# Performance work log

Measured on AMD Instinct MI355X. Metric: run time of the kernel, lower is better.

## Reference

```python
import jax, jax.numpy as jnp
import numpy as np

B, N, H, S = 64, 2048, 128, 8192
K, DEAD_K = 32, 8
BN_EPS = 1e-5


def _bn_train(x, gamma, beta):
    # BatchNorm1d training-mode math over (batch, length) per channel; x: [B,C,N]
    mean = jnp.mean(x, axis=(0, 2), keepdims=True)
    var = jnp.var(x, axis=(0, 2), keepdims=True)
    xh = (x - mean) * jax.lax.rsqrt(var + BN_EPS)
    return xh * gamma[None, :, None] + beta[None, :, None]


def setup_inputs() -> dict:
    key = jax.random.key(0)
    ks = jax.random.split(key, 20)

    def lin(k, out_d, in_d):
        s = 1.0 / np.sqrt(in_d)
        return jax.random.uniform(k, (out_d, in_d), jnp.float32, -s, s)

    def bias(k, d, fan_in):
        s = 1.0 / np.sqrt(fan_in)
        return jax.random.uniform(k, (d,), jnp.float32, -s, s)

    inp = {
        "pts": jax.random.normal(ks[0], (B, 3, N), jnp.float32),
        "dead_features": jax.random.randint(ks[1], (S,), 0, 10, jnp.int32),
        "conv1_w": lin(ks[2], 128, 3), "conv1_b": bias(ks[3], 128, 3),
        "conv2_w": lin(ks[4], 128, 128), "conv2_b": bias(ks[5], 128, 128),
        "conv3_w": lin(ks[6], 256, 128), "conv3_b": bias(ks[7], 256, 128),
        "conv4_w": lin(ks[8], 512, 256), "conv4_b": bias(ks[9], 512, 256),
        "bn1_g": jnp.ones(128), "bn1_b": jnp.zeros(128),
        "bn2_g": jnp.ones(128), "bn2_b": jnp.zeros(128),
        "bn3_g": jnp.ones(256), "bn3_b": jnp.zeros(256),
        "bn4_g": jnp.ones(512), "bn4_b": jnp.zeros(512),
        "fc1_w": lin(ks[10], 256, 512), "fc1_b": bias(ks[11], 256, 512),
        "fc2_w": lin(ks[12], H, 256), "fc2_b": bias(ks[13], H, 256),
        "sae2_w": lin(ks[14], H, S),  # sae1.weight = sae2.weight.T (tied init)
        "sae1_b": jnp.zeros(S), "sae2_b": jnp.zeros(H),
    }
    inp["sae1_w"] = inp["sae2_w"].T  # [S,H]
    return inp


def reference(pts, dead_features, conv1_w, conv1_b, conv2_w, conv2_b,
              conv3_w, conv3_b, conv4_w, conv4_b,
              bn1_g, bn1_b, bn2_g, bn2_b, bn3_g, bn3_b, bn4_g, bn4_b,
              fc1_w, fc1_b, fc2_w, fc2_b, sae2_w, sae1_b, sae2_b, sae1_w):
    def conv1x1(x, w, b):  # x:[B,Ci,N] w:[Co,Ci] -> [B,Co,N]
        return jnp.einsum('bcn,oc->bon', x, w) + b[None, :, None]

    h = jax.nn.relu(_bn_train(conv1x1(pts, conv1_w, conv1_b), bn1_g, bn1_b))
    h = jax.nn.relu(_bn_train(conv1x1(h, conv2_w, conv2_b), bn2_g, bn2_b))
    h = jax.nn.relu(_bn_train(conv1x1(h, conv3_w, conv3_b), bn3_g, bn3_b))
    h = _bn_train(conv1x1(h, conv4_w, conv4_b), bn4_g, bn4_b)
    h = jnp.max(h, axis=2)  # global max pool -> [B,512]
    h = jax.nn.relu(h @ fc1_w.T + fc1_b)
    x = jax.nn.relu(h @ fc2_w.T + fc2_b)  # hidden rep [B,H]

    # run_sae (stage 1, batch_topk=True)
    _x = x - sae2_b
    f = jax.nn.relu(_x @ sae1_w.T + sae1_b)  # [B,S]
    flat = f.reshape(-1)                     # [B*S]
    topk_vals, inds = jax.lax.top_k(flat, K * B)
    dead_mask = jnp.broadcast_to(dead_features >= 5, (B, S)).reshape(-1)
    dead_flat = jnp.where(dead_mask, flat, 0.0)
    dead_vals, dead_inds = jax.lax.top_k(dead_flat, DEAD_K * B)
    f_out = jnp.zeros_like(flat).at[inds].set(topk_vals).reshape(B, S)
    dead_f = jnp.zeros_like(flat).at[dead_inds].set(dead_vals).reshape(B, S)
    recon = f_out @ sae2_w.T + sae2_b
    dead_x = dead_f @ sae2_w.T + sae2_b
    return (x, recon, f_out, dead_x)
```

## Files before the change

kernel.cpp:

```cpp
#include <hip/hip_runtime.h>
#include <hip/hip_bf16.h>
#include <stdint.h>

#define B_   64
#define N_   2048
#define C1_  128
#define C2_  128
#define C3_  256
#define C4_  512
#define H_   128
#define S_   8192
#define KTOT 2048
#define DTOT 512
#define TIE_CAP 4096
#define BN_EPS 1e-5f
#define NPART 1024

#define I_PTS 0
#define I_DEAD 1
#define I_C1W 2
#define I_C1B 3
#define I_C2W 4
#define I_C2B 5
#define I_C3W 6
#define I_C3B 7
#define I_C4W 8
#define I_C4B 9
#define I_BN1G 10
#define I_BN1B 11
#define I_BN2G 12
#define I_BN2B 13
#define I_BN3G 14
#define I_BN3B 15
#define I_BN4G 16
#define I_BN4B 17
#define I_FC1W 18
#define I_FC1B 19
#define I_FC2W 20
#define I_FC2B 21
#define I_SAE2W 22
#define I_SAE1B 23
#define I_SAE2B 24
#define I_SAE1W 25

typedef const void* const* Tbl;
struct P26 { const void* p[26]; };

typedef _Float16 f16x8 __attribute__((ext_vector_type(8)));
typedef _Float16 f16x4 __attribute__((ext_vector_type(4)));
typedef float f32x16 __attribute__((ext_vector_type(16)));

__global__ void k_sentinel(float* outx, float v){
  if(threadIdx.x==0) outx[0] = v;
}

__global__ void k_route(P26 in, const void** tbl, int* flag){
  if(threadIdx.x != 0) return;
  const uint32_t* a   = (const uint32_t*)in.p[1];
  const uint32_t* g10 = (const uint32_t*)in.p[10];
  const uint32_t* d16 = (const uint32_t*)in.p[16];
  bool onesA  = a[0]==0x3F800000u && a[1]==0x3F800000u && a[2]==0x3F800000u && a[3]==0x3F800000u;
  bool intsA  = a[0]<=9u && a[1]<=9u && a[2]<=9u && a[3]<=9u;
  bool ones10 = g10[0]==0x3F800000u && g10[1]==0x3F800000u;
  bool ints16 = d16[0]<=9u && d16[1]<=9u;
  int f = 0;
  if(intsA && ones10) f = 1;
  else if(onesA && ints16) f = 2;
  const int permI[26] = {0,1,2,3,4,5,6,7,8,9,10,11,12,13,14,15,16,17,18,19,20,21,22,23,24,25};
  const int permA[26] = {21,16,9,8,11,10,13,12,15,14,1,0,3,2,5,4,7,6,18,17,20,19,25,22,24,23};
  const int* pm = (f==2) ? permA : permI;
  for(int i=0;i<26;i++) tbl[i] = in.p[pm[i]];
  *flag = f;
}

__global__ void k_init(uint32_t* ctrl, uint32_t* cnt, uint32_t* hist,
                       uint32_t* ctrl2, uint32_t* cnt2, uint32_t* hist2,
                       float* racc, float* dacc){
  int t = blockIdx.x*256 + threadIdx.x;
  if(t < 256){ hist[t]=0u; hist2[t]=0u; }
  if(t == 0){
    ctrl[0]=0u;  ctrl[1]=KTOT;  cnt[0]=0u;  cnt[1]=0u;  cnt[2]=0u;
    ctrl2[0]=0u; ctrl2[1]=DTOT; cnt2[0]=0u; cnt2[1]=0u; cnt2[2]=0u;
  }
  if(t < B_*H_){ racc[t]=0.f; dacc[t]=0.f; }
}

__global__ void k_mom(Tbl tbl, float* __restrict__ mom){
  const float* pts = (const float*)tbl[I_PTS];
  int b = blockIdx.x, t = threadIdx.x;
  const float* p0 = pts + (size_t)b*3*N_;
  const float* p1 = p0 + N_;
  const float* p2 = p1 + N_;
  float v[9] = {};
  for(int n=t;n<N_;n+=256){
    float a=p0[n], c=p1[n], d=p2[n];
    v[0]+=a; v[1]+=c; v[2]+=d;
    v[3]=fmaf(a,a,v[3]); v[4]=fmaf(a,c,v[4]); v[5]=fmaf(a,d,v[5]);
    v[6]=fmaf(c,c,v[6]); v[7]=fmaf(c,d,v[7]); v[8]=fmaf(d,d,v[8]);
  }
  __shared__ float red[256];
  for(int i=0;i<9;i++){
    red[t]=v[i]; __syncthreads();
    for(int off=128;off>0;off>>=1){ if(t<off) red[t]+=red[t+off]; __syncthreads(); }
    if(t==0) mom[b*16+i]=red[0];
    __syncthreads();
  }
}

__global__ void k_bn1fold(const float* __restrict__ mom, Tbl tbl, float* __restrict__ ew){
  const float* w1 = (const float*)tbl[I_C1W];
  const float* b1 = (const float*)tbl[I_C1B];
  const float* g  = (const float*)tbl[I_BN1G];
  const float* be = (const float*)tbl[I_BN1B];
  __shared__ float tot[9];
  int t = threadIdx.x;
  if(t < 9){
    float s=0.f;
    for(int b=0;b<B_;b++) s += mom[b*16+t];
    tot[t]=s;
  }
  __syncthreads();
  const float inv = 1.f/((float)B_*(float)N_);
  float mu0=tot[0]*inv, mu1=tot[1]*inv, mu2=tot[2]*inv;
  float M00=tot[3]*inv, M01=tot[4]*inv, M02=tot[5]*inv;
  float M11=tot[6]*inv, M12=tot[7]*inv, M22=tot[8]*inv;
  float w0=w1[t*3+0], ww1=w1[t*3+1], w2=w1[t*3+2];
  float bb=b1[t];
  float wmu = w0*mu0 + ww1*mu1 + w2*mu2;
  float m = wmu + bb;
  float E2 = w0*w0*M00 + ww1*ww1*M11 + w2*w2*M22
           + 2.f*(w0*ww1*M01 + w0*w2*M02 + ww1*w2*M12)
           + 2.f*bb*wmu + bb*bb;
  float var = E2 - m*m; if(var<0.f) var=0.f;
  float a = g[t] / sqrtf(var + BN_EPS);
  float sh = be[t] - m*a;
  ew[t*4+0]=a*w0; ew[t*4+1]=a*ww1; ew[t*4+2]=a*w2; ew[t*4+3]=fmaf(a,bb,sh);
}

template<int CI, int CO, int SRCP, int STOREY, int MM, int TILED>
__global__ __launch_bounds__(256)
void k_conv(const float* __restrict__ yin, Tbl tbl, int wi, int bi,
            const float* __restrict__ aAct, const float* __restrict__ bAct,
            float* __restrict__ yout,
            float* __restrict__ psum, float* __restrict__ psq,
            float* __restrict__ pmx, float* __restrict__ pmn){
  const float* W    = (const float*)tbl[wi];
  const float* bias = (const float*)tbl[bi];
  __shared__ float Ws[16][132];
  __shared__ float As[16][132];
  __shared__ float ps[3][128];
  const int b  = blockIdx.z;
  const int o0 = blockIdx.y*128;
  const int n0 = blockIdx.x*128;
  const int nt = blockIdx.x;
  const int t  = threadIdx.x;
  const int tx = t & 15, ty = t >> 4;
  const int wo = t >> 1;
  const int wk = (t & 1)*8;
  const int ar = t >> 4;
  const int an4 = (t & 15)*4;
  if(SRCP){
    const float* pts = (const float*)tbl[I_PTS];
    if(t < 48){
      int j = t >> 4, cc = (t & 15)*8;
      const float* pp = pts + ((size_t)b*3 + j)*N_ + n0 + cc;
      const float4 p0 = *(const float4*)pp;
      const float4 p1 = *(const float4*)(pp+4);
      ps[j][cc+0]=p0.x; ps[j][cc+1]=p0.y; ps[j][cc+2]=p0.z; ps[j][cc+3]=p0.w;
      ps[j][cc+4]=p1.x; ps[j][cc+5]=p1.y; ps[j][cc+6]=p1.z; ps[j][cc+7]=p1.w;
    }
    __syncthreads();
  }
  const float* ybase = SRCP ? (const float*)nullptr : (yin + (size_t)b*CI*N_);
  float acc[8][8] = {};
  for(int k0=0;k0<CI;k0+=16){
    {
      const float* wp = W + (size_t)(o0+wo)*CI + (k0+wk);
      const float4 wa = *(const float4*)wp;
      const float4 wb = *(const float4*)(wp+4);
      Ws[wk+0][wo]=wa.x; Ws[wk+1][wo]=wa.y; Ws[wk+2][wo]=wa.z; Ws[wk+3][wo]=wa.w;
      Ws[wk+4][wo]=wb.x; Ws[wk+5][wo]=wb.y; Ws[wk+6][wo]=wb.z; Ws[wk+7][wo]=wb.w;
    }
    {
      const int c = k0 + ar;
      float av[8];
      if(SRCP){
        const float e0=aAct[c*4+0], e1=aAct[c*4+1], e2=aAct[c*4+2], e3=aAct[c*4+3];
        #pragma unroll
        for(int x=0;x<4;x++){
          float v = fmaf(e0, ps[0][an4+x], fmaf(e1, ps[1][an4+x], fmaf(e2, ps[2][an4+x], e3)));
          av[x] = fmaxf(v, 0.f);
        }
        #pragma unroll
        for(int x=0;x<4;x++){
          float v = fmaf(e0, ps[0][64+an4+x], fmaf(e1, ps[1][64+an4+x], fmaf(e2, ps[2][64+an4+x], e3)));
          av[4+x] = fmaxf(v, 0.f);
        }
      } else {
        const float* yp = ybase + (size_t)c*N_ + n0;
        const float4 v0 = *(const float4*)(yp + an4);
        const float4 v1 = *(const float4*)(yp + 64 + an4);
        const float a = aAct[c], bb = bAct[c];
        av[0]=fmaxf(fmaf(a,v0.x,bb),0.f); av[1]=fmaxf(fmaf(a,v0.y,bb),0.f);
        av[2]=fmaxf(fmaf(a,v0.z,bb),0.f); av[3]=fmaxf(fmaf(a,v0.w,bb),0.f);
        av[4]=fmaxf(fmaf(a,v1.x,bb),0.f); av[5]=fmaxf(fmaf(a,v1.y,bb),0.f);
        av[6]=fmaxf(fmaf(a,v1.z,bb),0.f); av[7]=fmaxf(fmaf(a,v1.w,bb),0.f);
      }
      *(float4*)&As[ar][an4]    = make_float4(av[0],av[1],av[2],av[3]);
      *(float4*)&As[ar][64+an4] = make_float4(av[4],av[5],av[6],av[7]);
    }
    __syncthreads();
    #pragma unroll
    for(int kk=0;kk<16;kk++){
      const float4 w0 = *(const float4*)&Ws[kk][ty*8];
      const float4 w1 = *(const float4*)&Ws[kk][ty*8+4];
      const float4 a0 = *(const float4*)&As[kk][tx*4];
      const float4 a1 = *(const float4*)&As[kk][64+tx*4];
      const float wr[8] = {w0.x,w0.y,w0.z,w0.w,w1.x,w1.y,w1.z,w1.w};
      const float ac[8] = {a0.x,a0.y,a0.z,a0.w,a1.x,a1.y,a1.z,a1.w};
      #pragma unroll
      for(int i=0;i<8;i++)
        #pragma unroll
        for(int j=0;j<8;j++)
          acc[i][j] = fmaf(wr[i], ac[j], acc[i][j]);
    }
    __syncthreads();
  }
  float bo[8];
  #pragma unroll
  for(int i=0;i<8;i++) bo[i] = bias[o0 + ty*8 + i];
  if(STOREY && TILED){
    const int ks = (o0 + ty*8) >> 4;
    float* yb2 = yout + ((((size_t)(b*16 + nt))*(CO/16) + ks)*128)*16 + (ty&1)*8;
    #pragma unroll
    for(int jj=0;jj<8;jj++){
      const int nn = (jj<4) ? (tx*4 + jj) : (64 + tx*4 + (jj-4));
      float4 lo = make_float4(acc[0][jj]+bo[0], acc[1][jj]+bo[1],
                              acc[2][jj]+bo[2], acc[3][jj]+bo[3]);
      float4 hi = make_float4(acc[4][jj]+bo[4], acc[5][jj]+bo[5],
                              acc[6][jj]+bo[6], acc[7][jj]+bo[7]);
      *(float4*)(yb2 + (size_t)nn*16)     = lo;
      *(float4*)(yb2 + (size_t)nn*16 + 4) = hi;
    }
  }
  #pragma unroll
  for(int i=0;i<8;i++){
    const int o = o0 + ty*8 + i;
    float v[8];
    #pragma unroll
    for(int j=0;j<8;j++) v[j] = acc[i][j] + bo[i];
    if(STOREY && !TILED){
      float* yo = yout + ((size_t)b*CO + o)*N_ + n0;
      *(float4*)(yo + tx*4)      = make_float4(v[0],v[1],v[2],v[3]);
      *(float4*)(yo + 64 + tx*4) = make_float4(v[4],v[5],v[6],v[7]);
    }
    float s = 0.f, q = 0.f;
    #pragma unroll
    for(int j=0;j<8;j++){ s += v[j]; q = fmaf(v[j],v[j],q); }
    float mx=0.f, mn=0.f;
    if(MM){
      mx = v[0]; mn = v[0];
      #pragma unroll
      for(int j=1;j<8;j++){ mx = fmaxf(mx,v[j]); mn = fminf(mn,v[j]); }
    }
    #pragma unroll
    for(int m=1;m<16;m<<=1){
      s += __shfl_xor(s,m);
      q += __shfl_xor(q,m);
      if(MM){ mx = fmaxf(mx,__shfl_xor(mx,m)); mn = fminf(mn,__shfl_xor(mn,m)); }
    }
    if(tx==0){
      psum[(size_t)o*NPART + b*16 + nt] = s;
      psq [(size_t)o*NPART + b*16 + nt] = q;
      if(MM){
        pmx[((size_t)b*CO + o)*16 + nt] = mx;
        pmn[((size_t)b*CO + o)*16 + nt] = mn;
      }
    }
  }
}

__global__ void k_wcvt(Tbl tbl, _Float16* __restrict__ whi, _Float16* __restrict__ wlo){
  const float* W = (const float*)tbl[I_C4W];
  int u = blockIdx.x*256 + threadIdx.x;
  int h = u & 1, o_loc = (u>>1)&127, ks = (u>>8)&15, oy = u>>12;
  int o = oy*128 + o_loc;
  int c0 = ks*16 + h*8;
  const float* wp = W + (size_t)o*C3_ + c0;
  f16x8 vh, vl;
  #pragma unroll
  for(int j=0;j<8;j++){
    float w = wp[j]*1024.f;
    _Float16 hi = (_Float16)w;
    vh[j] = hi;
    vl[j] = (_Float16)(w - (float)hi);
  }
  int uo = (oy*16 + ks)*256 + (o_loc>>5)*64 + h*32 + (o_loc&31);
  *(f16x8*)(whi + (size_t)uo*8) = vh;
  *(f16x8*)(wlo + (size_t)uo*8) = vl;
}

__global__ void k_wcvt3(Tbl tbl, _Float16* __restrict__ whi, _Float16* __restrict__ wlo){
  const float* W = (const float*)tbl[I_C3W];
  int u = blockIdx.x*256 + threadIdx.x;
  int h = u & 1, o_loc = (u>>1)&127, ks = (u>>8)&7, oy = u>>11;
  int o = oy*128 + o_loc;
  int c0 = ks*16 + h*8;
  const float* wp = W + (size_t)o*C2_ + c0;
  f16x8 vh, vl;
  #pragma unroll
  for(int j=0;j<8;j++){
    float w = wp[j]*1024.f;
    _Float16 hi = (_Float16)w;
    vh[j] = hi;
    vl[j] = (_Float16)(w - (float)hi);
  }
  int uo = (oy*8 + ks)*256 + (o_loc>>5)*64 + h*32 + (o_loc&31);
  *(f16x8*)(whi + (size_t)uo*8) = vh;
  *(f16x8*)(wlo + (size_t)uo*8) = vl;
}

__global__ void k_t2(const float* __restrict__ y2t, const float* __restrict__ a2A,
                     const float* __restrict__ b2A,
                     _Float16* __restrict__ a2h, _Float16* __restrict__ a2l){
  int u = blockIdx.x*256 + threadIdx.x;
  int h = u & 1, nn = (u>>1)&127, ks = (u>>8)&7, tile = u>>11;
  int c0 = ks*16 + h*8;
  const float* yp = y2t + (size_t)u*8;
  f16x8 vh, vl;
  #pragma unroll
  for(int j=0;j<8;j++){
    float v = fmaxf(fmaf(a2A[c0+j], yp[j], b2A[c0+j]), 0.f);
    _Float16 hi = (_Float16)v;
    vh[j] = hi;
    vl[j] = (_Float16)(v - (float)hi);
  }
  int uo = (tile*8 + ks)*256 + (nn>>5)*64 + h*32 + (nn&31);
  *(f16x8*)(a2h + (size_t)uo*8) = vh;
  *(f16x8*)(a2l + (size_t)uo*8) = vl;
}

__global__ __launch_bounds__(256)
void k_conv3m(const _Float16* __restrict__ a2h, const _Float16* __restrict__ a2l,
              const _Float16* __restrict__ whi, const _Float16* __restrict__ wlo,
              Tbl tbl, _Float16* __restrict__ y3h, _Float16* __restrict__ y3l,
              float* __restrict__ psum, float* __restrict__ psq){
  const float* bias = (const float*)tbl[I_C3B];
  __shared__ float sred[2048];
  const int nt = blockIdx.x, oy = blockIdx.y, b = blockIdx.z;
  const int t = threadIdx.x, l = t & 63, w = t >> 6;
  const int wr = w >> 1, wc = w & 1, h = l >> 5, ln = l & 31;
  const char* gWh = (const char*)whi + (size_t)oy*32768 + wr*2048 + l*16;
  const char* gWl = (const char*)wlo + (size_t)oy*32768 + wr*2048 + l*16;
  const char* gAh = (const char*)a2h + (size_t)(b*16 + nt)*32768 + wc*2048 + l*16;
  const char* gAl = (const char*)a2l + (size_t)(b*16 + nt)*32768 + wc*2048 + l*16;
  f32x16 acc00 = {}, acc01 = {}, acc10 = {}, acc11 = {};
  f16x8 nwh0 = *(const f16x8*)(gWh);
  f16x8 nwh1 = *(const f16x8*)(gWh + 1024);
  f16x8 nwl0 = *(const f16x8*)(gWl);
  f16x8 nwl1 = *(const f16x8*)(gWl + 1024);
  f16x8 nbh0 = *(const f16x8*)(gAh);
  f16x8 nbh1 = *(const f16x8*)(gAh + 1024);
  f16x8 nbl0 = *(const f16x8*)(gAl);
  f16x8 nbl1 = *(const f16x8*)(gAl + 1024);
  #pragma unroll
  for(int ks=0; ks<8; ks++){
    f16x8 wh0 = nwh0, wh1 = nwh1, wl0 = nwl0, wl1 = nwl1;
    f16x8 bh0 = nbh0, bh1 = nbh1, bl0 = nbl0, bl1 = nbl1;
    if(ks < 7){
      const int o = (ks+1)*4096;
      nwh0 = *(const f16x8*)(gWh + o);
      nwh1 = *(const f16x8*)(gWh + o + 1024);
      nwl0 = *(const f16x8*)(gWl + o);
      nwl1 = *(const f16x8*)(gWl + o + 1024);
      nbh0 = *(const f16x8*)(gAh + o);
      nbh1 = *(const f16x8*)(gAh + o + 1024);
      nbl0 = *(const f16x8*)(gAl + o);
      nbl1 = *(const f16x8*)(gAl + o + 1024);
    }
    acc00 = __builtin_amdgcn_mfma_f32_32x32x16_f16(wh0, bh0, acc00, 0,0,0);
    acc00 = __builtin_amdgcn_mfma_f32_32x32x16_f16(wl0, bh0, acc00, 0,0,0);
    acc00 = __builtin_amdgcn_mfma_f32_32x32x16_f16(wh0, bl0, acc00, 0,0,0);
    acc01 = __builtin_amdgcn_mfma_f32_32x32x16_f16(wh0, bh1, acc01, 0,0,0);
    acc01 = __builtin_amdgcn_mfma_f32_32x32x16_f16(wl0, bh1, acc01, 0,0,0);
    acc01 = __builtin_amdgcn_mfma_f32_32x32x16_f16(wh0, bl1, acc01, 0,0,0);
    acc10 = __builtin_amdgcn_mfma_f32_32x32x16_f16(wh1, bh0, acc10, 0,0,0);
    acc10 = __builtin_amdgcn_mfma_f32_32x32x16_f16(wl1, bh0, acc10, 0,0,0);
    acc10 = __builtin_amdgcn_mfma_f32_32x32x16_f16(wh1, bl0, acc10, 0,0,0);
    acc11 = __builtin_amdgcn_mfma_f32_32x32x16_f16(wh1, bh1, acc11, 0,0,0);
    acc11 = __builtin_amdgcn_mfma_f32_32x32x16_f16(wl1, bh1, acc11, 0,0,0);
    acc11 = __builtin_amdgcn_mfma_f32_32x32x16_f16(wh1, bl1, acc11, 0,0,0);
  }
  float* Ss = sred;
  float* Sq = Ss + 1024;
  const float inv = 1.f/1024.f;
  const int o0 = oy*128;
  const int grp = ln >> 3;
  const int tile = b*16 + nt;
  #pragma unroll
  for(int to=0; to<2; to++){
    const f32x16 a0 = to ? acc10 : acc00;
    const f32x16 a1 = to ? acc11 : acc01;
    f16x4 p0h, p1h, p0l, p1l;
    #pragma unroll
    for(int r=0; r<16; r++){
      const int row = (r&3) + 8*(r>>2) + 4*h;
      const int ol = wr*64 + to*32 + row;
      const float bo = bias[o0 + ol];
      float v0 = fmaf(a0[r], inv, bo);
      float v1 = fmaf(a1[r], inv, bo);
      _Float16 h0 = (_Float16)v0, h1 = (_Float16)v1;
      p0h[r&3] = h0; p1h[r&3] = h1;
      p0l[r&3] = (_Float16)(v0 - (float)h0);
      p1l[r&3] = (_Float16)(v1 - (float)h1);
      if((r&3) == 3){
        const int o3 = o0 + wr*64 + to*32 + 8*(r>>2) + 4*h;
        const int ks3 = o3 >> 4, kk = o3 & 15;
        const int n0c = wc*64 + ln;
        const size_t rb = ((size_t)(tile*16 + ks3))*128;
        *(f16x4*)(y3h + (rb + n0c)*16 + kk)      = p0h;
        *(f16x4*)(y3h + (rb + n0c + 32)*16 + kk) = p1h;
        *(f16x4*)(y3l + (rb + n0c)*16 + kk)      = p0l;
        *(f16x4*)(y3l + (rb + n0c + 32)*16 + kk) = p1l;
      }
      float s = v0 + v1;
      float q = fmaf(v0, v0, v1*v1);
      #pragma unroll
      for(int m=1; m<8; m<<=1){
        s += __shfl_xor(s, m);
        q += __shfl_xor(q, m);
      }
      if((ln & 7) == 0){
        const int idx = (wc*4 + grp)*128 + ol;
        Ss[idx] = s;  Sq[idx] = q;
      }
    }
  }
  __syncthreads();
  if(t < 128){
    const int o = o0 + t;
    float s = 0.f, q = 0.f;
    #pragma unroll
    for(int g=0; g<8; g++){
      s += Ss[g*128 + t];
      q += Sq[g*128 + t];
    }
    psum[(size_t)o*NPART + b*16 + nt] = s;
    psq [(size_t)o*NPART + b*16 + nt] = q;
  }
}

__global__ void k_t3(const _Float16* __restrict__ y3h, const _Float16* __restrict__ y3l,
                     const float* __restrict__ a3, const float* __restrict__ b3,
                     _Float16* __restrict__ a4){
  int u = blockIdx.x*256 + threadIdx.x;
  int h = u & 1, nn = (u>>1)&127, ks = (u>>8)&15, tile = u>>12;
  int c0 = ks*16 + h*8;
  const f16x8 yh = *(const f16x8*)(y3h + (size_t)u*8);
  const f16x8 yl = *(const f16x8*)(y3l + (size_t)u*8);
  f16x8 vh;
  #pragma unroll
  for(int j=0;j<8;j++){
    float y = (float)yh[j] + (float)yl[j];
    float v = fmaxf(fmaf(a3[c0+j], y, b3[c0+j]), 0.f);
    vh[j] = (_Float16)v;
  }
  int uo = (tile*16 + ks)*256 + (nn>>5)*64 + h*32 + (nn&31);
  *(f16x8*)(a4 + (size_t)uo*8) = vh;
}

__global__ __launch_bounds__(256)
void k_conv4m(const _Float16* __restrict__ a4,
              const _Float16* __restrict__ whi, const _Float16* __restrict__ wlo,
              Tbl tbl,
              float* __restrict__ psum, float* __restrict__ psq,
              float* __restrict__ pmx, float* __restrict__ pmn){
  const float* bias = (const float*)tbl[I_C4B];
  __shared__ float sred[4096];
  const int nt = blockIdx.x, oy = blockIdx.y, b = blockIdx.z;
  const int t = threadIdx.x, l = t & 63, w = t >> 6;
  const int wr = w >> 1, wc = w & 1, h = l >> 5, ln = l & 31;
  const char* gWh = (const char*)whi + (size_t)oy*65536 + wr*2048 + l*16;
  const char* gWl = (const char*)wlo + (size_t)oy*65536 + wr*2048 + l*16;
  const char* gA  = (const char*)a4  + (size_t)(b*16 + nt)*65536 + wc*2048 + l*16;
  f32x16 acc00 = {}, acc01 = {}, acc10 = {}, acc11 = {};
  f16x8 nah0 = *(const f16x8*)(gWh);
  f16x8 nah1 = *(const f16x8*)(gWh + 1024);
  f16x8 nal0 = *(const f16x8*)(gWl);
  f16x8 nal1 = *(const f16x8*)(gWl + 1024);
  f16x8 nb0  = *(const f16x8*)(gA);
  f16x8 nb1  = *(const f16x8*)(gA + 1024);
  #pragma unroll
  for(int ks=0; ks<16; ks++){
    f16x8 ah0 = nah0, ah1 = nah1, al0 = nal0, al1 = nal1;
    f16x8 b0  = nb0,  b1  = nb1;
    if(ks < 15){
      const int o = (ks+1)*4096;
      nah0 = *(const f16x8*)(gWh + o);
      nah1 = *(const f16x8*)(gWh + o + 1024);
      nal0 = *(const f16x8*)(gWl + o);
      nal1 = *(const f16x8*)(gWl + o + 1024);
      nb0  = *(const f16x8*)(gA  + o);
      nb1  = *(const f16x8*)(gA  + o + 1024);
    }
    acc00 = __builtin_amdgcn_mfma_f32_32x32x16_f16(ah0, b0, acc00, 0,0,0);
    acc00 = __builtin_amdgcn_mfma_f32_32x32x16_f16(al0, b0, acc00, 0,0,0);
    acc01 = __builtin_amdgcn_mfma_f32_32x32x16_f16(ah0, b1, acc01, 0,0,0);
    acc01 = __builtin_amdgcn_mfma_f32_32x32x16_f16(al0, b1, acc01, 0,0,0);
    acc10 = __builtin_amdgcn_mfma_f32_32x32x16_f16(ah1, b0, acc10, 0,0,0);
    acc10 = __builtin_amdgcn_mfma_f32_32x32x16_f16(al1, b0, acc10, 0,0,0);
    acc11 = __builtin_amdgcn_mfma_f32_32x32x16_f16(ah1, b1, acc11, 0,0,0);
    acc11 = __builtin_amdgcn_mfma_f32_32x32x16_f16(al1, b1, acc11, 0,0,0);
  }
  float* Ss = sred;
  float* Sq = Ss + 1024;
  float* Sx = Sq + 1024;
  float* Sn = Sx + 1024;
  const float inv = 1.f/1024.f;
  const int o0 = oy*128;
  const int grp = ln >> 3;
  #pragma unroll
  for(int to=0; to<2; to++){
    const f32x16 a0 = to ? acc10 : acc00;
    const f32x16 a1 = to ? acc11 : acc01;
    #pragma unroll
    for(int r=0; r<16; r++){
      const int row = (r&3) + 8*(r>>2) + 4*h;
      const int ol = wr*64 + to*32 + row;
      const float bo = bias[o0 + ol];
      float v0 = fmaf(a0[r], inv, bo);
      float v1 = fmaf(a1[r], inv, bo);
      float s = v0 + v1;
      float q = fmaf(v0, v0, v1*v1);
      float mx = fmaxf(v0, v1), mn = fminf(v0, v1);
      #pragma unroll
      for(int m=1; m<8; m<<=1){
        s += __shfl_xor(s, m);
        q += __shfl_xor(q, m);
        mx = fmaxf(mx, __shfl_xor(mx, m));
        mn = fminf(mn, __shfl_xor(mn, m));
      }
      if((ln & 7) == 0){
        const int idx = (wc*4 + grp)*128 + ol;
        Ss[idx] = s;  Sq[idx] = q;
        Sx[idx] = mx; Sn[idx] = mn;
      }
    }
  }
  __syncthreads();
  if(t < 128){
    const int o = o0 + t;
    float s = 0.f, q = 0.f;
    float mx = -__builtin_inff(), mn = __builtin_inff();
    #pragma unroll
    for(int g=0; g<8; g++){
      s += Ss[g*128 + t];
      q += Sq[g*128 + t];
      mx = fmaxf(mx, Sx[g*128 + t]);
      mn = fminf(mn, Sn[g*128 + t]);
    }
    psum[(size_t)o*NPART + b*16 + nt] = s;
    psq [(size_t)o*NPART + b*16 + nt] = q;
    pmx[((size_t)b*C4_ + o)*16 + nt] = mx;
    pmn[((size_t)b*C4_ + o)*16 + nt] = mn;
  }
}

__global__ void k_finalize(const float* __restrict__ psum, const float* __restrict__ psq,
                           Tbl tbl, int gi, int bi,
                           float* __restrict__ aout, float* __restrict__ bout){
  const float* gamma = (const float*)tbl[gi];
  const float* beta  = (const float*)tbl[bi];
  int c = blockIdx.x, t = threadIdx.x;
  float s=0.f, q=0.f;
  for(int i=t;i<NPART;i+=256){ s+=psum[(size_t)c*NPART+i]; q+=psq[(size_t)c*NPART+i]; }
  __shared__ float ls[256], lq[256];
  ls[t]=s; lq[t]=q; __syncthreads();
  for(int off=128; off>0; off>>=1){
    if(t<off){ ls[t]+=ls[t+off]; lq[t]+=lq[t+off]; }
    __syncthreads();
  }
  if(t==0){
    const float cnt = (float)B_*(float)N_;
    float mean = ls[0]/cnt;
    float var  = lq[0]/cnt - mean*mean;
    if(var < 0.f) var = 0.f;
    float a = gamma[c] / sqrtf(var + BN_EPS);
    aout[c] = a;
    bout[c] = beta[c] - mean*a;
  }
}

__global__ void k_pool(const float* __restrict__ pmx, const float* __restrict__ pmn,
                       const float* __restrict__ aA, const float* __restrict__ bA,
                       float* __restrict__ pooled){
  int idx = blockIdx.x*256 + threadIdx.x;
  int o = idx & (C4_-1);
  float mx=-__builtin_inff(), mn=__builtin_inff();
  for(int k=0;k<16;k++){
    mx = fmaxf(mx, pmx[(size_t)idx*16+k]);
    mn = fminf(mn, pmn[(size_t)idx*16+k]);
  }
  float a=aA[o], bb=bA[o];
  pooled[idx] = (a>=0.f) ? fmaf(a,mx,bb) : fmaf(a,mn,bb);
}

__global__ void k_fc1(const float* __restrict__ pooled, Tbl tbl, float* __restrict__ out){
  const float* w    = (const float*)tbl[I_FC1W];
  const float* bias = (const float*)tbl[I_FC1B];
  __shared__ float xp[512];
  int b = blockIdx.x, t = threadIdx.x;
  for(int i=t;i<512;i+=256) xp[i] = pooled[(size_t)b*512+i];
  __syncthreads();
  const float* wr = w + (size_t)t*512;
  float acc = 0.f;
  for(int c=0;c<512;c++) acc = fmaf(xp[c], wr[c], acc);
  out[(size_t)b*256 + t] = fmaxf(acc + bias[t], 0.f);
}

__global__ void k_fc2(const float* __restrict__ in, Tbl tbl,
                      float* __restrict__ xbuf, float* __restrict__ xout){
  const float* w    = (const float*)tbl[I_FC2W];
  const float* bias = (const float*)tbl[I_FC2B];
  __shared__ float xp[256];
  int b = blockIdx.x, t = threadIdx.x;
  for(int i=t;i<256;i+=128) xp[i] = in[(size_t)b*256+i];
  __syncthreads();
  const float* wr = w + (size_t)t*256;
  float acc = 0.f;
  for(int c=0;c<256;c++) acc = fmaf(xp[c], wr[c], acc);
  float v = fmaxf(acc + bias[t], 0.f);
  xbuf[(size_t)b*H_ + t] = v;
  xout[(size_t)b*H_ + t] = v;
}

__global__ void k_sae(const float* __restrict__ xbuf, Tbl tbl, float* __restrict__ f){
  const float* w  = (const float*)tbl[I_SAE1W];
  const float* b1 = (const float*)tbl[I_SAE1B];
  const float* b2 = (const float*)tbl[I_SAE2B];
  __shared__ float xp[H_];
  int b = blockIdx.y, t = threadIdx.x;
  if(t < H_) xp[t] = xbuf[(size_t)b*H_ + t] - b2[t];
  __syncthreads();
  int s = blockIdx.x*256 + t;
  const float* wr = w + (size_t)s*H_;
  float acc = 0.f;
  for(int h=0;h<H_;h++) acc = fmaf(xp[h], wr[h], acc);
  acc += b1[s];
  f[(size_t)b*S_ + s] = fmaxf(acc, 0.f);
}

__global__ void k_hist(const float* __restrict__ f, Tbl tbl,
                       int mode, int shift, const uint32_t* __restrict__ ctrl,
                       uint32_t* __restrict__ hist){
  const int* df = (const int*)tbl[I_DEAD];
  __shared__ uint32_t lh[256];
  int t = threadIdx.x;
  lh[t] = 0u; __syncthreads();
  const uint32_t prefix = ctrl[0];
  const uint32_t mask = (shift == 24) ? 0u : (0xFFFFFFFFu << (shift+8));
  int i0 = blockIdx.x*1024 + t;
  #pragma unroll
  for(int j=0;j<4;j++){
    int i = i0 + j*256;
    float v = f[i];
    if(mode){ int s = i & (S_-1); if(df[s] < 5) v = 0.f; }
    uint32_t u = __float_as_uint(v);
    if((u & mask) == prefix) atomicAdd(&lh[(u>>shift)&255u], 1u);
  }
  __syncthreads();
  if(lh[t]) atomicAdd(&hist[t], lh[t]);
}

__global__ void k_scan(uint32_t* ctrl, uint32_t* hist, int shift){
  if(threadIdx.x == 0){
    uint32_t rem = ctrl[1];
    uint32_t cum = 0; int tb = 0;
    for(int bin=255; bin>=0; bin--){
      uint32_t c = hist[bin];
      if(cum + c >= rem){ tb = bin; rem = rem - cum; break; }
      cum += c;
    }
    ctrl[0] |= ((uint32_t)tb) << shift;
    ctrl[1] = rem;
  }
  __syncthreads();
  hist[threadIdx.x] = 0u;
}

__global__ void k_select(const float* __restrict__ f, Tbl tbl,
                         int mode, int kcap, const uint32_t* __restrict__ ctrl,
                         uint32_t* __restrict__ cnt, uint32_t* __restrict__ sel,
                         uint32_t* __restrict__ tie){
  const int* df = (const int*)tbl[I_DEAD];
  int i = blockIdx.x*256 + threadIdx.x;
  float v = f[i];
  if(mode){ int s = i & (S_-1); if(df[s] < 5) v = 0.f; }
  uint32_t u = __float_as_uint(v);
  const uint32_t T = ctrl[0];
  if(u > T){ uint32_t p = atomicAdd(&cnt[0], 1u); if(p < (uint32_t)kcap) sel[p] = (uint32_t)i; }
  else if(u == T){ uint32_t p = atomicAdd(&cnt[1], 1u); if(p < TIE_CAP) tie[p] = (uint32_t)i; }
}

__global__ void k_resolve(const uint32_t* __restrict__ ctrl, uint32_t* __restrict__ cnt,
                          uint32_t* __restrict__ sel, const uint32_t* __restrict__ tie,
                          int kcap){
  if(threadIdx.x != 0) return;
  uint32_t m = ctrl[1];
  uint32_t ngt = cnt[0]; if(ngt > (uint32_t)kcap) ngt = (uint32_t)kcap;
  uint32_t ntie = cnt[1]; if(ntie > TIE_CAP) ntie = TIE_CAP;
  uint32_t last = 0u; bool first = true;
  for(uint32_t it=0; it<m; it++){
    uint32_t best = 0xFFFFFFFFu;
    for(uint32_t j=0;j<ntie;j++){
      uint32_t v = tie[j];
      if((first || v > last) && v < best) best = v;
    }
    if(best == 0xFFFFFFFFu) break;
    if(ngt + it < (uint32_t)kcap) sel[ngt + it] = best;
    last = best; first = false;
  }
  uint32_t tot = ngt + m; if(tot > (uint32_t)kcap) tot = (uint32_t)kcap;
  cnt[2] = tot;
}

__global__ void k_scatter(const uint32_t* __restrict__ sel, const uint32_t* __restrict__ cnt,
                          const float* __restrict__ f, float* __restrict__ fout){
  uint32_t t = blockIdx.x*256 + threadIdx.x;
  if(t >= cnt[2]) return;
  uint32_t i = sel[t];
  if(i < (uint32_t)(B_*S_)) fout[i] = f[i];
}

__global__ void k_accum(const uint32_t* __restrict__ sel, const uint32_t* __restrict__ cnt,
                        const float* __restrict__ f, Tbl tbl, int mode,
                        float* __restrict__ acc){
  const int* df = (const int*)tbl[I_DEAD];
  const float* w2 = (const float*)tbl[I_SAE2W];
  uint32_t e = blockIdx.x;
  if(e >= cnt[2]) return;
  uint32_t i = sel[e];
  if(i >= (uint32_t)(B_*S_)) return;
  uint32_t b = i >> 13, s = i & (S_-1);
  float v = f[i];
  if(mode && df[s] < 5) v = 0.f;
  int h = threadIdx.x;
  float wv = w2[(size_t)h*S_ + s];
  atomicAdd(&acc[b*H_ + h], v*wv);
}

__global__ void k_final(const float* __restrict__ racc, const float* __restrict__ dacc,
                        Tbl tbl, float* __restrict__ outR, float* __restrict__ outD){
  const float* b2 = (const float*)tbl[I_SAE2B];
  int idx = blockIdx.x*256 + threadIdx.x;
  int h = idx & (H_-1);
  float bb = b2[h];
  outR[idx] = racc[idx] + bb;
  outD[idx] = dacc[idx] + bb;
}

__global__ void k_health(const int* __restrict__ flag, const float* __restrict__ xb,
                         float* __restrict__ outx){
  __shared__ float red[256];
  int t = threadIdx.x;
  float s = 0.f;
  for(int i=t;i<B_*H_;i+=256) s += fabsf(xb[i]);
  red[t]=s; __syncthreads();
  for(int off=128;off>0;off>>=1){ if(t<off) red[t]+=red[t+off]; __syncthreads(); }
  if(t==0){
    float avg = red[0]/(float)(B_*H_);
    int f = *flag;
    float v = 0.f;
    if(f == 0) v = 12000.f;
    else if(!(avg >= 0.05f && avg <= 50.f)) v = 40000.f + 1000.f*(float)f;
    if(v > 0.f) outx[0] = v;
  }
}

extern "C" void kernel_launch(void* const* d_in, const int* in_sizes, int n_in,
                              void* d_out, int out_size, void* d_ws, size_t ws_size,
                              hipStream_t stream){
  (void)in_sizes; (void)n_in;
  float* out       = (float*)d_out;
  float* out_x     = out;
  float* out_recon = out + 8192;
  float* out_fout  = out + 16384;
  float* out_deadx = out + 540672;

  char* p = (char*)d_ws;
  auto take = [&](size_t bytes)->char*{
    char* r = p; p += (bytes + 255) & ~(size_t)255; return r;
  };
  float* y2   = (float*)take((size_t)B_*C2_*N_*4);
  float* y3   = (float*)take((size_t)B_*C3_*N_*4);
  float* psum = (float*)take((size_t)C4_*NPART*4);
  float* psq  = (float*)take((size_t)C4_*NPART*4);
  float* pmx  = (float*)take((size_t)B_*C4_*16*4);
  float* pmn  = (float*)take((size_t)B_*C4_*16*4);
  float* mom  = (float*)take(64*16*4);
  float* ab   = (float*)take(4096*4);
  float* pooled=(float*)take((size_t)B_*C4_*4);
  float* fc1o = (float*)take((size_t)B_*256*4);
  float* xb   = (float*)take((size_t)B_*H_*4);
  float* fb   = (float*)take((size_t)B_*S_*4);
  float* racc = (float*)take((size_t)B_*H_*4);
  float* dacc = (float*)take((size_t)B_*H_*4);
  uint32_t* hist  = (uint32_t*)take(256*4);
  uint32_t* ctrl  = (uint32_t*)take(64);
  uint32_t* cnt   = (uint32_t*)take(64);
  uint32_t* sel   = (uint32_t*)take((size_t)KTOT*4);
  uint32_t* tie   = (uint32_t*)take((size_t)TIE_CAP*4);
  uint32_t* hist2 = (uint32_t*)take(256*4);
  uint32_t* ctrl2 = (uint32_t*)take(64);
  uint32_t* cnt2  = (uint32_t*)take(64);
  uint32_t* sel2  = (uint32_t*)take((size_t)DTOT*4);
  uint32_t* tie2  = (uint32_t*)take((size_t)TIE_CAP*4);
  const void** tbl = (const void**)take(32*sizeof(void*));
  int* flag = (int*)take(64);
  size_t need = (size_t)(p - (char*)d_ws);
  _Float16* y3hi = (_Float16*)y3;
  _Float16* y3lo = (_Float16*)y2;
  _Float16* a2h  = (_Float16*)((char*)y3 + 67108864);
  _Float16* a2l  = (_Float16*)((char*)y3 + 100663296);
  _Float16* a4   = (_Float16*)((char*)y3 + 67108864);
  _Float16* w4hi = (_Float16*)fb;
  _Float16* w4lo = (_Float16*)((char*)fb + 262144);
  _Float16* w3hi = (_Float16*)((char*)fb + 524288);
  _Float16* w3lo = (_Float16*)((char*)fb + 589824);

  hipMemsetAsync(d_out, 0, (size_t)out_size*sizeof(float), stream);
  if(ws_size != 0 && ws_size < need){
    k_sentinel<<<1,64,0,stream>>>(out_x, 15000.f);
    return;
  }

  P26 ptrs;
  for(int i=0;i<26;i++) ptrs.p[i] = d_in[i];
  k_route<<<1,64,0,stream>>>(ptrs, tbl, flag);
  k_init<<<32,256,0,stream>>>(ctrl,cnt,hist,ctrl2,cnt2,hist2,racc,dacc);

  k_mom<<<B_,256,0,stream>>>(tbl,mom);
  k_bn1fold<<<1,128,0,stream>>>(mom,tbl,ab);
  k_wcvt<<<64,256,0,stream>>>(tbl, w4hi, w4lo);
  k_wcvt3<<<16,256,0,stream>>>(tbl, w3hi, w3lo);

  k_conv<C1_,C2_,1,1,0,1><<<dim3(N_/128,C2_/128,B_),256,0,stream>>>(
      nullptr,tbl,I_C2W,I_C2B,ab,nullptr,y2,psum,psq,nullptr,nullptr);
  k_finalize<<<C2_,256,0,stream>>>(psum,psq,tbl,I_BN2G,I_BN2B,ab+512,ab+640);
  k_t2<<<8192,256,0,stream>>>(y2, ab+512, ab+640, a2h, a2l);
  k_conv3m<<<dim3(16,2,64),256,0,stream>>>(a2h, a2l, w3hi, w3lo, tbl,
                                           y3hi, y3lo, psum, psq);
  k_finalize<<<C3_,256,0,stream>>>(psum,psq,tbl,I_BN3G,I_BN3B,ab+768,ab+1024);
  k_t3<<<16384,256,0,stream>>>(y3hi, y3lo, ab+768, ab+1024, a4);
  k_conv4m<<<dim3(16,4,64),256,0,stream>>>(a4, w4hi, w4lo, tbl,
                                           psum, psq, pmx, pmn);
  k_finalize<<<C4_,256,0,stream>>>(psum,psq,tbl,I_BN4G,I_BN4B,ab+1280,ab+1792);
  k_pool<<<(B_*C4_)/256,256,0,stream>>>(pmx,pmn,ab+1280,ab+1792,pooled);

  k_fc1<<<B_,256,0,stream>>>(pooled,tbl,fc1o);
  k_fc2<<<B_,128,0,stream>>>(fc1o,tbl,xb,out_x);
  k_sae<<<dim3(S_/256,B_),256,0,stream>>>(xb,tbl,fb);

  for(int pass=0;pass<4;pass++){
    int shift = 24 - 8*pass;
    k_hist<<<512,256,0,stream>>>(fb,tbl,0,shift,ctrl,hist);
    k_scan<<<1,256,0,stream>>>(ctrl,hist,shift);
  }
  k_select<<<2048,256,0,stream>>>(fb,tbl,0,KTOT,ctrl,cnt,sel,tie);
  k_resolve<<<1,64,0,stream>>>(ctrl,cnt,sel,tie,KTOT);
  k_scatter<<<8,256,0,stream>>>(sel,cnt,fb,out_fout);
  k_accum<<<KTOT,128,0,stream>>>(sel,cnt,fb,tbl,0,racc);

  for(int pass=0;pass<4;pass++){
    int shift = 24 - 8*pass;
    k_hist<<<512,256,0,stream>>>(fb,tbl,1,shift,ctrl2,hist2);
    k_scan<<<1,256,0,stream>>>(ctrl2,hist2,shift);
  }
  k_select<<<2048,256,0,stream>>>(fb,tbl,1,DTOT,ctrl2,cnt2,sel2,tie2);
  k_resolve<<<1,64,0,stream>>>(ctrl2,cnt2,sel2,tie2,DTOT);
  k_accum<<<DTOT,128,0,stream>>>(sel2,cnt2,fb,tbl,1,dacc);

  k_final<<<(B_*H_)/256,256,0,stream>>>(racc,dacc,tbl,out_recon,out_deadx);

  k_health<<<1,256,0,stream>>>(flag,xb,out_x);
}
```

Baseline: 668.1 us.

## Fuse pool/fc head and run both top-k selections in shared passes

Merges the pool, fc1 and fc2 kernels into one per-batch head kernel, so the intermediate pooled and fc1 buffers no longer round-trip through global memory. The two radix-select top-k pipelines (regular and dead-feature) now run together: each histogram, scan, select, resolve and accumulate kernel handles both selections, and the scatter into f_out is folded into the accumulate kernel. This roughly halves the number of small launches and passes over the 2M-element activation buffer. In exchange each fused kernel does more work per element and uses more atomics and shared memory.

```diff
diff --git a/kernel.cpp b/kernel.cpp
--- a/kernel.cpp
+++ b/kernel.cpp
@@ -591,47 +591,44 @@
   }
 }
 
-__global__ void k_pool(const float* __restrict__ pmx, const float* __restrict__ pmn,
-                       const float* __restrict__ aA, const float* __restrict__ bA,
-                       float* __restrict__ pooled){
-  int idx = blockIdx.x*256 + threadIdx.x;
-  int o = idx & (C4_-1);
-  float mx=-__builtin_inff(), mn=__builtin_inff();
-  for(int k=0;k<16;k++){
-    mx = fmaxf(mx, pmx[(size_t)idx*16+k]);
-    mn = fminf(mn, pmn[(size_t)idx*16+k]);
-  }
-  float a=aA[o], bb=bA[o];
-  pooled[idx] = (a>=0.f) ? fmaf(a,mx,bb) : fmaf(a,mn,bb);
-}
-
-__global__ void k_fc1(const float* __restrict__ pooled, Tbl tbl, float* __restrict__ out){
-  const float* w    = (const float*)tbl[I_FC1W];
-  const float* bias = (const float*)tbl[I_FC1B];
+__global__ __launch_bounds__(256)
+void k_head(const float* __restrict__ pmx, const float* __restrict__ pmn,
+            const float* __restrict__ aA, const float* __restrict__ bA,
+            Tbl tbl, float* __restrict__ xbuf, float* __restrict__ xout){
+  const float* w1    = (const float*)tbl[I_FC1W];
+  const float* b1    = (const float*)tbl[I_FC1B];
+  const float* w2    = (const float*)tbl[I_FC2W];
+  const float* b2    = (const float*)tbl[I_FC2B];
   __shared__ float xp[512];
+  __shared__ float fo[256];
   int b = blockIdx.x, t = threadIdx.x;
-  for(int i=t;i<512;i+=256) xp[i] = pooled[(size_t)b*512+i];
+  for(int o = t; o < 512; o += 256){
+    const size_t idx = (size_t)(b*512 + o);
+    float mx=-__builtin_inff(), mn=__builtin_inff();
+    #pragma unroll
+    for(int k=0;k<16;k++){
+      mx = fmaxf(mx, pmx[idx*16+k]);
+      mn = fminf(mn, pmn[idx*16+k]);
+    }
+    float a=aA[o], bb=bA[o];
+    xp[o] = (a>=0.f) ? fmaf(a,mx,bb) : fmaf(a,mn,bb);
+  }
   __syncthreads();
-  const float* wr = w + (size_t)t*512;
-  float acc = 0.f;
-  for(int c=0;c<512;c++) acc = fmaf(xp[c], wr[c], acc);
-  out[(size_t)b*256 + t] = fmaxf(acc + bias[t], 0.f);
-}
-
-__global__ void k_fc2(const float* __restrict__ in, Tbl tbl,
-                      float* __restrict__ xbuf, float* __restrict__ xout){
-  const float* w    = (const float*)tbl[I_FC2W];
-  const float* bias = (const float*)tbl[I_FC2B];
-  __shared__ float xp[256];
-  int b = blockIdx.x, t = threadIdx.x;
-  for(int i=t;i<256;i+=128) xp[i] = in[(size_t)b*256+i];
+  {
+    const float* wr = w1 + (size_t)t*512;
+    float acc = 0.f;
+    for(int c=0;c<512;c++) acc = fmaf(xp[c], wr[c], acc);
+    fo[t] = fmaxf(acc + b1[t], 0.f);
+  }
   __syncthreads();
-  const float* wr = w + (size_t)t*256;
-  float acc = 0.f;
-  for(int c=0;c<256;c++) acc = fmaf(xp[c], wr[c], acc);
-  float v = fmaxf(acc + bias[t], 0.f);
-  xbuf[(size_t)b*H_ + t] = v;
-  xout[(size_t)b*H_ + t] = v;
+  if(t < 128){
+    const float* wr = w2 + (size_t)t*256;
+    float acc = 0.f;
+    for(int c=0;c<256;c++) acc = fmaf(fo[c], wr[c], acc);
+    float v = fmaxf(acc + b2[t], 0.f);
+    xbuf[(size_t)b*H_ + t] = v;
+    xout[(size_t)b*H_ + t] = v;
+  }
 }
 
 __global__ void k_sae(const float* __restrict__ xbuf, Tbl tbl, float* __restrict__ f){
@@ -650,62 +647,73 @@
   f[(size_t)b*S_ + s] = fmaxf(acc, 0.f);
 }
 
-__global__ void k_hist(const float* __restrict__ f, Tbl tbl,
-                       int mode, int shift, const uint32_t* __restrict__ ctrl,
-                       uint32_t* __restrict__ hist){
+__global__ void k_hist2(const float* __restrict__ f, Tbl tbl, int shift,
+                        const uint32_t* __restrict__ ctrl,  uint32_t* __restrict__ hist,
+                        const uint32_t* __restrict__ ctrl2, uint32_t* __restrict__ hist2){
   const int* df = (const int*)tbl[I_DEAD];
-  __shared__ uint32_t lh[256];
+  __shared__ uint32_t lh[256], lh2[256];
   int t = threadIdx.x;
-  lh[t] = 0u; __syncthreads();
-  const uint32_t prefix = ctrl[0];
+  lh[t] = 0u; lh2[t] = 0u; __syncthreads();
+  const uint32_t p1 = ctrl[0], p2 = ctrl2[0];
   const uint32_t mask = (shift == 24) ? 0u : (0xFFFFFFFFu << (shift+8));
   int i0 = blockIdx.x*1024 + t;
   #pragma unroll
   for(int j=0;j<4;j++){
     int i = i0 + j*256;
     float v = f[i];
-    if(mode){ int s = i & (S_-1); if(df[s] < 5) v = 0.f; }
     uint32_t u = __float_as_uint(v);
-    if((u & mask) == prefix) atomicAdd(&lh[(u>>shift)&255u], 1u);
+    if((u & mask) == p1) atomicAdd(&lh[(u>>shift)&255u], 1u);
+    int s = i & (S_-1);
+    uint32_t ud = (df[s] < 5) ? 0u : u;
+    if((ud & mask) == p2) atomicAdd(&lh2[(ud>>shift)&255u], 1u);
   }
   __syncthreads();
-  if(lh[t]) atomicAdd(&hist[t], lh[t]);
-}
-
-__global__ void k_scan(uint32_t* ctrl, uint32_t* hist, int shift){
-  if(threadIdx.x == 0){
-    uint32_t rem = ctrl[1];
-    uint32_t cum = 0; int tb = 0;
-    for(int bin=255; bin>=0; bin--){
-      uint32_t c = hist[bin];
-      if(cum + c >= rem){ tb = bin; rem = rem - cum; break; }
-      cum += c;
-    }
-    ctrl[0] |= ((uint32_t)tb) << shift;
-    ctrl[1] = rem;
-  }
+  if(lh[t])  atomicAdd(&hist[t],  lh[t]);
+  if(lh2[t]) atomicAdd(&hist2[t], lh2[t]);
+}
+
+__device__ void scan1(uint32_t* ctrl, const uint32_t* hist, int shift){
+  uint32_t rem = ctrl[1];
+  uint32_t cum = 0; int tb = 0;
+  for(int bin=255; bin>=0; bin--){
+    uint32_t c = hist[bin];
+    if(cum + c >= rem){ tb = bin; rem = rem - cum; break; }
+    cum += c;
+  }
+  ctrl[0] |= ((uint32_t)tb) << shift;
+  ctrl[1] = rem;
+}
+
+__global__ void k_scan2(uint32_t* ctrl, uint32_t* hist,
+                        uint32_t* ctrl2, uint32_t* hist2, int shift){
+  int t = threadIdx.x;
+  if(t == 0)  scan1(ctrl,  hist,  shift);
+  if(t == 64) scan1(ctrl2, hist2, shift);
   __syncthreads();
-  hist[threadIdx.x] = 0u;
-}
-
-__global__ void k_select(const float* __restrict__ f, Tbl tbl,
-                         int mode, int kcap, const uint32_t* __restrict__ ctrl,
-                         uint32_t* __restrict__ cnt, uint32_t* __restrict__ sel,
-                         uint32_t* __restrict__ tie){
+  hist[t] = 0u; hist2[t] = 0u;
+}
+
+__global__ void k_select2(const float* __restrict__ f, Tbl tbl,
+                          const uint32_t* __restrict__ ctrl,  uint32_t* __restrict__ cnt,
+                          uint32_t* __restrict__ sel,  uint32_t* __restrict__ tie,
+                          const uint32_t* __restrict__ ctrl2, uint32_t* __restrict__ cnt2,
+                          uint32_t* __restrict__ sel2, uint32_t* __restrict__ tie2){
   const int* df = (const int*)tbl[I_DEAD];
   int i = blockIdx.x*256 + threadIdx.x;
   float v = f[i];
-  if(mode){ int s = i & (S_-1); if(df[s] < 5) v = 0.f; }
   uint32_t u = __float_as_uint(v);
   const uint32_t T = ctrl[0];
-  if(u > T){ uint32_t p = atomicAdd(&cnt[0], 1u); if(p < (uint32_t)kcap) sel[p] = (uint32_t)i; }
+  if(u > T){ uint32_t p = atomicAdd(&cnt[0], 1u); if(p < (uint32_t)KTOT) sel[p] = (uint32_t)i; }
   else if(u == T){ uint32_t p = atomicAdd(&cnt[1], 1u); if(p < TIE_CAP) tie[p] = (uint32_t)i; }
-}
-
-__global__ void k_resolve(const uint32_t* __restrict__ ctrl, uint32_t* __restrict__ cnt,
-                          uint32_t* __restrict__ sel, const uint32_t* __restrict__ tie,
-                          int kcap){
-  if(threadIdx.x != 0) return;
+  int s = i & (S_-1);
+  uint32_t ud = (df[s] < 5) ? 0u : u;
+  const uint32_t T2 = ctrl2[0];
+  if(ud > T2){ uint32_t p = atomicAdd(&cnt2[0], 1u); if(p < (uint32_t)DTOT) sel2[p] = (uint32_t)i; }
+  else if(ud == T2){ uint32_t p = atomicAdd(&cnt2[1], 1u); if(p < TIE_CAP) tie2[p] = (uint32_t)i; }
+}
+
+__device__ void resolve1(const uint32_t* ctrl, uint32_t* cnt, uint32_t* sel,
+                         const uint32_t* tie, int kcap){
   uint32_t m = ctrl[1];
   uint32_t ngt = cnt[0]; if(ngt > (uint32_t)kcap) ngt = (uint32_t)kcap;
   uint32_t ntie = cnt[1]; if(ntie > TIE_CAP) ntie = TIE_CAP;
@@ -724,26 +732,37 @@
   cnt[2] = tot;
 }
 
-__global__ void k_scatter(const uint32_t* __restrict__ sel, const uint32_t* __restrict__ cnt,
-                          const float* __restrict__ f, float* __restrict__ fout){
-  uint32_t t = blockIdx.x*256 + threadIdx.x;
-  if(t >= cnt[2]) return;
-  uint32_t i = sel[t];
-  if(i < (uint32_t)(B_*S_)) fout[i] = f[i];
-}
-
-__global__ void k_accum(const uint32_t* __restrict__ sel, const uint32_t* __restrict__ cnt,
-                        const float* __restrict__ f, Tbl tbl, int mode,
-                        float* __restrict__ acc){
+__global__ void k_resolve2(const uint32_t* __restrict__ ctrl,  uint32_t* __restrict__ cnt,
+                           uint32_t* __restrict__ sel,  const uint32_t* __restrict__ tie,
+                           const uint32_t* __restrict__ ctrl2, uint32_t* __restrict__ cnt2,
+                           uint32_t* __restrict__ sel2, const uint32_t* __restrict__ tie2){
+  int t = threadIdx.x;
+  if(t == 0)  resolve1(ctrl,  cnt,  sel,  tie,  KTOT);
+  if(t == 64) resolve1(ctrl2, cnt2, sel2, tie2, DTOT);
+}
+
+__global__ void k_accum2(const uint32_t* __restrict__ sel,  const uint32_t* __restrict__ cnt,
+                         const uint32_t* __restrict__ sel2, const uint32_t* __restrict__ cnt2,
+                         const float* __restrict__ f, Tbl tbl,
+                         float* __restrict__ racc, float* __restrict__ dacc,
+                         float* __restrict__ fout){
   const int* df = (const int*)tbl[I_DEAD];
   const float* w2 = (const float*)tbl[I_SAE2W];
   uint32_t e = blockIdx.x;
-  if(e >= cnt[2]) return;
-  uint32_t i = sel[e];
-  if(i >= (uint32_t)(B_*S_)) return;
-  uint32_t b = i >> 13, s = i & (S_-1);
-  float v = f[i];
+  int mode; uint32_t idx; float* acc;
+  if(e < (uint32_t)KTOT){
+    if(e >= cnt[2]) return;
+    idx = sel[e]; mode = 0; acc = racc;
+  } else {
+    e -= (uint32_t)KTOT;
+    if(e >= cnt2[2]) return;
+    idx = sel2[e]; mode = 1; acc = dacc;
+  }
+  if(idx >= (uint32_t)(B_*S_)) return;
+  uint32_t b = idx >> 13, s = idx & (S_-1);
+  float v = f[idx];
   if(mode && df[s] < 5) v = 0.f;
+  if(mode == 0 && threadIdx.x == 0) fout[idx] = v;
   int h = threadIdx.x;
   float wv = w2[(size_t)h*S_ + s];
   atomicAdd(&acc[b*H_ + h], v*wv);
@@ -818,6 +837,7 @@
   const void** tbl = (const void**)take(32*sizeof(void*));
   int* flag = (int*)take(64);
   size_t need = (size_t)(p - (char*)d_ws);
+  (void)pooled; (void)fc1o;
   _Float16* y3hi = (_Float16*)y3;
   _Float16* y3lo = (_Float16*)y2;
   _Float16* a2h  = (_Float16*)((char*)y3 + 67108864);
@@ -855,30 +875,18 @@
   k_conv4m<<<dim3(16,4,64),256,0,stream>>>(a4, w4hi, w4lo, tbl,
                                            psum, psq, pmx, pmn);
   k_finalize<<<C4_,256,0,stream>>>(psum,psq,tbl,I_BN4G,I_BN4B,ab+1280,ab+1792);
-  k_pool<<<(B_*C4_)/256,256,0,stream>>>(pmx,pmn,ab+1280,ab+1792,pooled);
-
-  k_fc1<<<B_,256,0,stream>>>(pooled,tbl,fc1o);
-  k_fc2<<<B_,128,0,stream>>>(fc1o,tbl,xb,out_x);
+
+  k_head<<<B_,256,0,stream>>>(pmx,pmn,ab+1280,ab+1792,tbl,xb,out_x);
   k_sae<<<dim3(S_/256,B_),256,0,stream>>>(xb,tbl,fb);
 
   for(int pass=0;pass<4;pass++){
     int shift = 24 - 8*pass;
-    k_hist<<<512,256,0,stream>>>(fb,tbl,0,shift,ctrl,hist);
-    k_scan<<<1,256,0,stream>>>(ctrl,hist,shift);
-  }
-  k_select<<<2048,256,0,stream>>>(fb,tbl,0,KTOT,ctrl,cnt,sel,tie);
-  k_resolve<<<1,64,0,stream>>>(ctrl,cnt,sel,tie,KTOT);
-  k_scatter<<<8,256,0,stream>>>(sel,cnt,fb,out_fout);
-  k_accum<<<KTOT,128,0,stream>>>(sel,cnt,fb,tbl,0,racc);
-
-  for(int pass=0;pass<4;pass++){
-    int shift = 24 - 8*pass;
-    k_hist<<<512,256,0,stream>>>(fb,tbl,1,shift,ctrl2,hist2);
-    k_scan<<<1,256,0,stream>>>(ctrl2,hist2,shift);
-  }
-  k_select<<<2048,256,0,stream>>>(fb,tbl,1,DTOT,ctrl2,cnt2,sel2,tie2);
-  k_resolve<<<1,64,0,stream>>>(ctrl2,cnt2,sel2,tie2,DTOT);
-  k_accum<<<DTOT,128,0,stream>>>(sel2,cnt2,fb,tbl,1,dacc);
+    k_hist2<<<512,256,0,stream>>>(fb,tbl,shift,ctrl,hist,ctrl2,hist2);
+    k_scan2<<<1,256,0,stream>>>(ctrl,hist,ctrl2,hist2,shift);
+  }
+  k_select2<<<2048,256,0,stream>>>(fb,tbl,ctrl,cnt,sel,tie,ctrl2,cnt2,sel2,tie2);
+  k_resolve2<<<1,128,0,stream>>>(ctrl,cnt,sel,tie,ctrl2,cnt2,sel2,tie2);
+  k_accum2<<<KTOT+DTOT,128,0,stream>>>(sel,cnt,sel2,cnt2,fb,tbl,racc,dacc,out_fout);
 
   k_final<<<(B_*H_)/256,256,0,stream>>>(racc,dacc,tbl,out_recon,out_deadx);
 
```

After: 614.1 us. -8.1%, faster.
